# Optimization experiments

Hardware: AMD Instinct MI355X
Metric: run time of the kernel (lower is better)

Reference implementation:

```python
import jax, jax.numpy as jnp
import numpy as np

B = 16384           # number of visits (segments)
EMB = 128           # embedding dim (hardcoded in module)
HID = 64            # hidden layer size
DIAG_LEN, PROC_LEN, MED_LEN = 2000, 1500, 153


def setup_inputs() -> dict:
    key = jax.random.key(0)
    ks = jax.random.split(key, 12)
    diag_codes = jax.random.randint(ks[0], (262144,), 0, DIAG_LEN)
    diag_seg = jnp.sort(jax.random.randint(ks[1], (262144,), 0, B))
    proc_codes = jax.random.randint(ks[2], (131072,), 0, PROC_LEN)
    proc_seg = jnp.sort(jax.random.randint(ks[3], (131072,), 0, B))
    med_codes = jax.random.randint(ks[4], (196608,), 0, MED_LEN)
    med_seg = jnp.sort(jax.random.randint(ks[5], (196608,), 0, B))
    diag_table = jax.random.normal(ks[6], (DIAG_LEN, EMB), dtype=jnp.float32)
    proc_table = jax.random.normal(ks[7], (PROC_LEN, EMB), dtype=jnp.float32)
    med_table = jax.random.normal(ks[8], (MED_LEN, EMB), dtype=jnp.float32)
    W1 = jax.random.normal(ks[9], (3 * EMB, HID), dtype=jnp.float32) * 0.05
    b1 = jnp.zeros((HID,), dtype=jnp.float32)
    W2 = jax.random.normal(ks[10], (HID, MED_LEN), dtype=jnp.float32) * 0.1
    b2 = jnp.zeros((MED_LEN,), dtype=jnp.float32)
    return {
        "diag_codes": diag_codes, "diag_seg": diag_seg,
        "proc_codes": proc_codes, "proc_seg": proc_seg,
        "med_codes": med_codes, "med_seg": med_seg,
        "diag_table": diag_table, "proc_table": proc_table, "med_table": med_table,
        "W1": W1, "b1": b1, "W2": W2, "b2": b2,
    }


def _embed_sum(table, codes, seg):
    # gather [N, EMB] then segment-sum to [B, EMB] (== per-visit sum of embeddings)
    return jax.ops.segment_sum(table[codes], seg, num_segments=B)


def reference(diag_codes, diag_seg, proc_codes, proc_seg, med_codes, med_seg,
              diag_table, proc_table, med_table, W1, b1, W2, b2):
    e_diag = _embed_sum(diag_table, diag_codes, diag_seg)   # [B, 128]
    e_proc = _embed_sum(proc_table, proc_codes, proc_seg)   # [B, 128]
    e_med = _embed_sum(med_table, med_codes, med_seg)       # [B, 128]
    x = jnp.concatenate([e_diag, e_proc, e_med], axis=1)    # [B, 384]
    h = jax.nn.relu(x @ W1 + b1)                            # [B, 64]
    return jax.nn.sigmoid(h @ W2 + b2)                      # [B, med_len]
```

## Files before the change

kernel.cpp:

```cpp
#include <hip/hip_runtime.h>
#include <hip/hip_bf16.h>

#define NVIS 16384
#define EMB 128
#define HID 64
#define MED 153
#define K1 384

#define ROWS_D 2000
#define ROWS_P 1500
#define ROWS_M 153
#define RT 3653
#define TBASE_D 0
#define TBASE_P 2000
#define TBASE_M 3500
#define E8S (RT * 16)

#define W2F_OFF  0u
#define OFFS_OFF 20480u
#define OFFS_STRIDE 16388
#define TW_OFF   217136u
#define H_OFF    684720u
#define WS_NEED  (684720u + 2097152u)

#define TWB_D 500
#define TWB_P 375
#define TWB_M 39
#define TWB_ALL (TWB_D + TWB_P + TWB_M)
#define NW2F 1280

typedef float f32x4 __attribute__((ext_vector_type(4)));
typedef short s16x8 __attribute__((ext_vector_type(8)));
typedef unsigned int u32;
typedef unsigned int u32x4 __attribute__((ext_vector_type(4)));

__device__ __forceinline__ unsigned short f2bf(float f) {
  union { float f; unsigned u; } v; v.f = f;
  unsigned r = v.u + 0x7FFFu + ((v.u >> 16) & 1u);
  return (unsigned short)(r >> 16);
}

__device__ __forceinline__ void acc8m(u32x4 t, float m, float* A) {
  union { unsigned u; float f; } c;
  c.u = t[0] << 16;          A[0] = fmaf(m, c.f, A[0]);
  c.u = t[0] & 0xFFFF0000u;  A[1] = fmaf(m, c.f, A[1]);
  c.u = t[1] << 16;          A[2] = fmaf(m, c.f, A[2]);
  c.u = t[1] & 0xFFFF0000u;  A[3] = fmaf(m, c.f, A[3]);
  c.u = t[2] << 16;          A[4] = fmaf(m, c.f, A[4]);
  c.u = t[2] & 0xFFFF0000u;  A[5] = fmaf(m, c.f, A[5]);
  c.u = t[3] << 16;          A[6] = fmaf(m, c.f, A[6]);
  c.u = t[3] & 0xFFFF0000u;  A[7] = fmaf(m, c.f, A[7]);
}

__device__ __forceinline__ int lb_scalar(const int* __restrict__ a, int lo, int hi, int key) {
  while (lo < hi) {
    int mid = (lo + hi) >> 1;
    if (a[mid] < key) lo = mid + 1; else hi = mid;
  }
  return lo;
}

__device__ __forceinline__ int lb_fast_scalar(const int* __restrict__ a, int n, int key) {
  long long g = ((long long)key * (long long)n) >> 14;
  int L = (int)g - 3072, R = (int)g + 3072;
  if (L < 0) L = 0;
  if (R > n) R = n;
  const bool ok = (L == 0 || a[L - 1] < key) && (R == n || a[R] >= key);
  if (!ok) { L = 0; R = n; }
  return lb_scalar(a, L, R, key);
}

__device__ __forceinline__ int lb_wave(const int* __restrict__ a, int n, int key, int lane) {
  long long g = ((long long)key * (long long)n) >> 14;
  int L = (int)g - 3072, R = (int)g + 3072;
  if (L < 0) L = 0;
  if (R > n) R = n;
  const bool ok = (L == 0 || a[L - 1] < key) && (R == n || a[R] >= key);
  if (!ok) { L = 0; R = n; }
  int lo = L - 1, hi = R;
  while (hi - lo > 1) {
    const int width = hi - lo - 1;
    const int p = lo + 1 + (int)(((long long)width * lane) >> 6);
    const bool lt = a[p] < key;
    const unsigned long long m = __ballot(lt);
    const int t = m ? (63 - __builtin_clzll(m)) : -1;
    const int nlo = (t >= 0) ? lo + 1 + (int)(((long long)width * t) >> 6) : lo;
    const int nhi = (t < 63) ? lo + 1 + (int)(((long long)width * (t + 1)) >> 6) : hi;
    lo = nlo; hi = nhi;
  }
  return hi;
}

__global__ __launch_bounds__(256, 4) void prep_kernel(
    const int* __restrict__ diag_seg, const int* __restrict__ proc_seg,
    const int* __restrict__ med_seg,
    const float* __restrict__ dT, const float* __restrict__ pT, const float* __restrict__ mT,
    const float* __restrict__ W1, const float* __restrict__ W2,
    unsigned char* __restrict__ ws, int ND, int NP, int NM)
{
  __shared__ float w1L[128 * 64];
  const int blk = blockIdx.x;
  const int tid = threadIdx.x;
  const int totSlots = ND + NP + NM + 3;
  const int SB = (totSlots + 255) >> 8;

  if (blk < SB) {
    const int t = blk * 256 + tid;
    if (t < totSlots) {
      int T, i, n; const int* seg;
      if (t < ND + 1)           { T = 0; i = t;                 n = ND; seg = diag_seg; }
      else if (t < ND + NP + 2) { T = 1; i = t - (ND + 1);      n = NP; seg = proc_seg; }
      else                      { T = 2; i = t - (ND + NP + 2); n = NM; seg = med_seg; }
      const int prev = (i == 0) ? -1 : seg[i - 1];
      const int cur  = (i == n) ? NVIS : seg[i];
      int* o = (int*)(ws + OFFS_OFF) + T * OFFS_STRIDE;
      for (int k = prev + 1; k <= cur; ++k) o[k] = i;
    }
  } else if (blk < SB + TWB_ALL) {
    const int blk2 = blk - SB;
    const float* tbl; int rows, r0, koff, tBase;
    if (blk2 < TWB_D)              { tbl = dT; rows = ROWS_D; r0 = blk2 * 4;           koff = 0;   tBase = TBASE_D; }
    else if (blk2 < TWB_D + TWB_P) { tbl = pT; rows = ROWS_P; r0 = (blk2 - TWB_D) * 4; koff = 128; tBase = TBASE_P; }
    else                           { tbl = mT; rows = ROWS_M; r0 = (blk2 - TWB_D - TWB_P) * 4; koff = 256; tBase = TBASE_M; }
    for (int i = tid; i < 128 * 64 / 4; i += 256)
      *(f32x4*)&w1L[i * 4] = *(const f32x4*)&W1[(size_t)koff * HID + i * 4];
    __syncthreads();
    const int r = r0 + (tid >> 6);
    const int j = tid & 63;
    if (r < rows) {
      float acc = 0.f;
      #pragma unroll 8
      for (int k4 = 0; k4 < 32; ++k4) {
        const f32x4 t = *(const f32x4*)(tbl + (size_t)r * EMB + k4 * 4);
        acc += t[0] * w1L[(k4 * 4 + 0) * 64 + j] + t[1] * w1L[(k4 * 4 + 1) * 64 + j]
             + t[2] * w1L[(k4 * 4 + 2) * 64 + j] + t[3] * w1L[(k4 * 4 + 3) * 64 + j];
      }
      *(unsigned short*)(ws + TW_OFF + (size_t)(j >> 3) * E8S
                         + (size_t)(tBase + r) * 16 + (size_t)(j & 7) * 2) = f2bf(acc);
    }
  } else {
    const int t = (blk - SB - TWB_ALL) * 256 + tid;
    if (t < NW2F) {
      const int lane = t & 63, tk = t >> 6;
      const int kh = tk & 1, tile = tk >> 1;
      const int n = tile * 16 + (lane & 15);
      const int k0 = kh * 32 + (lane >> 4) * 8;
      unsigned short e0[8];
      #pragma unroll
      for (int e = 0; e < 8; ++e)
        e0[e] = (n < MED) ? f2bf(W2[(size_t)(k0 + e) * MED + n]) : (unsigned short)0;
      u32x4 o;
      o[0] = (u32)e0[0] | ((u32)e0[1] << 16);
      o[1] = (u32)e0[2] | ((u32)e0[3] << 16);
      o[2] = (u32)e0[4] | ((u32)e0[5] << 16);
      o[3] = (u32)e0[6] | ((u32)e0[7] << 16);
      *(u32x4*)(ws + W2F_OFF + (size_t)t * 16) = o;
    }
  }
}

__global__ __launch_bounds__(1024, 8) void gather8_kernel(
    const int* __restrict__ diag_codes, const int* __restrict__ proc_codes,
    const int* __restrict__ med_codes,
    const float* __restrict__ b1,
    unsigned char* __restrict__ ws)
{
  __shared__ __align__(16) u32x4 twL[RT];
  __shared__ int offsB[3][257];

  const int tid = threadIdx.x;
  const int e8 = blockIdx.x >> 6;
  const int v0 = (blockIdx.x & 63) * 256;

  const unsigned char* src = ws + TW_OFF + (size_t)e8 * E8S;
  for (int k = tid; k < RT; k += 1024)
    twL[k] = *(const u32x4*)(src + (size_t)k * 16);
  const int* offsAll = (const int*)(ws + OFFS_OFF);
  for (int t = tid; t < 3 * 257; t += 1024) {
    const int T = (t < 257) ? 0 : (t < 514) ? 1 : 2;
    const int idx = t - T * 257;
    offsB[T][idx] = offsAll[T * OFFS_STRIDE + v0 + idx];
  }
  __syncthreads();

  const int v = tid >> 2;
  const int l4 = tid & 3;
  float A[8] = {0.f, 0.f, 0.f, 0.f, 0.f, 0.f, 0.f, 0.f};

#define G8(T, CG, TBASE)                                                    \
  {                                                                         \
    const int s = offsB[T][v], e = offsB[T][v + 1];                         \
    for (int i = s + l4; i < e; i += 8) {                                   \
      const int j1 = i + 4;                                                 \
      const int i1 = (j1 < e) ? j1 : (e - 1);                               \
      const int c0 = TBASE + CG[i];                                         \
      const int c1 = TBASE + CG[i1];                                        \
      const u32x4 t0 = twL[c0];                                             \
      const u32x4 t1 = twL[c1];                                             \
      acc8m(t0, 1.f, A);                                                    \
      acc8m(t1, (j1 < e) ? 1.f : 0.f, A);                                   \
    }                                                                       \
  }
  G8(0, diag_codes, TBASE_D)
  G8(1, proc_codes, TBASE_P)
  G8(2, med_codes,  TBASE_M)
#undef G8

  #pragma unroll
  for (int d = 0; d < 8; ++d) {
    A[d] += __shfl_xor(A[d], 1);
    A[d] += __shfl_xor(A[d], 2);
  }
  if (l4 == 0) {
    const f32x4 bb0 = *(const f32x4*)(b1 + e8 * 8);
    const f32x4 bb1 = *(const f32x4*)(b1 + e8 * 8 + 4);
    u32x4 o;
    o[0] = (u32)f2bf(fmaxf(A[0] + bb0[0], 0.f)) | ((u32)f2bf(fmaxf(A[1] + bb0[1], 0.f)) << 16);
    o[1] = (u32)f2bf(fmaxf(A[2] + bb0[2], 0.f)) | ((u32)f2bf(fmaxf(A[3] + bb0[3], 0.f)) << 16);
    o[2] = (u32)f2bf(fmaxf(A[4] + bb1[0], 0.f)) | ((u32)f2bf(fmaxf(A[5] + bb1[1], 0.f)) << 16);
    o[3] = (u32)f2bf(fmaxf(A[6] + bb1[2], 0.f)) | ((u32)f2bf(fmaxf(A[7] + bb1[3], 0.f)) << 16);
    *(u32x4*)(ws + H_OFF + (size_t)(v0 + v) * 128 + e8 * 16) = o;
  }
}

__global__ __launch_bounds__(256, 8) void mlp2_kernel(
    const unsigned char* __restrict__ ws,
    const float* __restrict__ b2, float* __restrict__ out)
{
  const int tid = threadIdx.x;
  const int l = tid & 63;
  const int wv = tid >> 6;
  const int jloc = l & 15;
  const int kq = l >> 4;
  const int m0 = blockIdx.x * 16;
  const unsigned char* h = ws + H_OFF;
  const s16x8* w2f = (const s16x8*)(ws + W2F_OFF);

  const s16x8 a00 = *(const s16x8*)(h + (size_t)(m0 + jloc) * 128 + kq * 16);
  const s16x8 a01 = *(const s16x8*)(h + (size_t)(m0 + jloc) * 128 + 64 + kq * 16);

  for (int t = wv; t < 10; t += 4) {
    const int n = t * 16 + jloc;
    const bool nok = (n < MED);
    const s16x8 bw0 = w2f[(t * 2 + 0) * 64 + l];
    const s16x8 bw1 = w2f[(t * 2 + 1) * 64 + l];
    f32x4 o0 = {0.f, 0.f, 0.f, 0.f};
    o0 = __builtin_amdgcn_mfma_f32_16x16x32_bf16(a00, bw0, o0, 0, 0, 0);
    o0 = __builtin_amdgcn_mfma_f32_16x16x32_bf16(a01, bw1, o0, 0, 0, 0);
    if (nok) {
      const float bias2 = b2[n];
      #pragma unroll
      for (int r = 0; r < 4; ++r) {
        const int row = kq * 4 + r;
        const float z0 = o0[r] + bias2;
        out[(size_t)(m0 + row) * MED + n] = 1.f / (1.f + __expf(-z0));
      }
    }
  }
}

#define VPB 16
#define NTHR 512
#define NBLK (NVIS / VPB)
#define CAPD 640
#define CAPP 384
#define CAPM 512
#define CAPT_FB (CAPD + CAPP + CAPM)

__global__ __launch_bounds__(NTHR, 8) void fused_ehr_fb(
    const int* __restrict__ diag_codes, const int* __restrict__ diag_seg,
    const int* __restrict__ proc_codes, const int* __restrict__ proc_seg,
    const int* __restrict__ med_codes,  const int* __restrict__ med_seg,
    const float* __restrict__ diag_table, const float* __restrict__ proc_table,
    const float* __restrict__ med_table,
    const float* __restrict__ W1, const float* __restrict__ b1,
    const float* __restrict__ W2, const float* __restrict__ b2,
    float* __restrict__ out, int ND, int NP, int NM)
{
  __shared__ __align__(16) unsigned short xs[VPB][K1 + 8];
  __shared__ __align__(16) unsigned short hs[VPB][HID + 8];
  __shared__ int offs[3][VPB + 1];
  __shared__ int codesL[CAPT_FB];

  const int tid = threadIdx.x;
  const int l = tid & 63;
  const int wv = tid >> 6;
  const int b0 = blockIdx.x * VPB;

  if (wv < 6) {
    const int T = wv >> 1, w = wv & 1;
    const int* seg = (T == 0) ? diag_seg : (T == 1) ? proc_seg : med_seg;
    const int n = (T == 0) ? ND : (T == 1) ? NP : NM;
    const int r = lb_wave(seg, n, b0 + (w ? VPB : 0), l);
    if (l == 0) offs[T][w ? VPB : 0] = r;
  }
  __syncthreads();

  const int sD = offs[0][0], cntD = offs[0][VPB] - sD;
  const int sP = offs[1][0], cntP = offs[1][VPB] - sP;
  const int sM = offs[2][0], cntM = offs[2][VPB] - sM;
  const bool stD = (cntD <= CAPD), stP = (cntP <= CAPP), stM = (cntM <= CAPM);

  if (tid < 3 * (VPB - 1)) {
    const int T = tid / (VPB - 1), idx = tid - T * (VPB - 1) + 1;
    offs[T][idx] = offs[T][VPB];
  }
  if (stD) for (int i = tid; i < cntD; i += NTHR) codesL[i] = diag_codes[sD + i];
  if (stP) for (int i = tid; i < cntP; i += NTHR) codesL[CAPD + i] = proc_codes[sP + i];
  if (stM) for (int i = tid; i < cntM; i += NTHR) codesL[CAPD + CAPP + i] = med_codes[sM + i];
  __syncthreads();

#define MARK(Tidx, STAGED, CNT, SBASE, SEGG, NT)                                 \
  if (STAGED) {                                                                  \
    for (int i = tid; i < CNT; i += NTHR) {                                      \
      const int v1 = SEGG[SBASE + i];                                            \
      const int v0_ = (i == 0) ? (b0 - 1) : SEGG[SBASE + i - 1];                 \
      int klo = v0_ + 1; if (klo < b0 + 1) klo = b0 + 1;                         \
      int khi = v1;      if (khi > b0 + VPB - 1) khi = b0 + VPB - 1;             \
      for (int k = klo; k <= khi; ++k) offs[Tidx][k - b0] = SBASE + i;           \
    }                                                                            \
  } else if (tid < VPB - 1) {                                                    \
    offs[Tidx][tid + 1] = lb_fast_scalar(SEGG, NT, b0 + tid + 1);                \
  }

  MARK(0, stD, cntD, sD, diag_seg, ND)
  MARK(1, stP, cntP, sP, proc_seg, NP)
  MARK(2, stM, cntM, sM, med_seg,  NM)
#undef MARK
  __syncthreads();

  const int half = tid >> 5;
  const int ln = tid & 31;

#define GATH(T, CODES_G, TBL, STAGED, SGLOB, LBASE)                               \
  {                                                                               \
    const int s_ = offs[T][half], e_ = offs[T][half + 1];                         \
    float a0 = 0.f, a1 = 0.f, a2 = 0.f, a3 = 0.f;                                 \
    int i = s_;                                                                   \
    if (STAGED) {                                                                 \
      const int lb = LBASE - SGLOB;                                               \
      for (; i + 3 < e_; i += 4) {                                                \
        const int c0 = codesL[lb + i],     c1 = codesL[lb + i + 1];               \
        const int c2 = codesL[lb + i + 2], c3 = codesL[lb + i + 3];               \
        const f32x4 t0 = *(const f32x4*)(TBL + (size_t)c0 * EMB + ln * 4);        \
        const f32x4 t1 = *(const f32x4*)(TBL + (size_t)c1 * EMB + ln * 4);        \
        const f32x4 t2 = *(const f32x4*)(TBL + (size_t)c2 * EMB + ln * 4);        \
        const f32x4 t3 = *(const f32x4*)(TBL + (size_t)c3 * EMB + ln * 4);        \
        a0 += (t0[0] + t1[0]) + (t2[0] + t3[0]);                                  \
        a1 += (t0[1] + t1[1]) + (t2[1] + t3[1]);                                  \
        a2 += (t0[2] + t1[2]) + (t2[2] + t3[2]);                                  \
        a3 += (t0[3] + t1[3]) + (t2[3] + t3[3]);                                  \
      }                                                                           \
      for (; i < e_; ++i) {                                                       \
        const int c = codesL[lb + i];                                             \
        const f32x4 t = *(const f32x4*)(TBL + (size_t)c * EMB + ln * 4);          \
        a0 += t[0]; a1 += t[1]; a2 += t[2]; a3 += t[3];                           \
      }                                                                           \
    } else {                                                                      \
      for (; i < e_; ++i) {                                                       \
        const int c = CODES_G[i];                                                 \
        const f32x4 t = *(const f32x4*)(TBL + (size_t)c * EMB + ln * 4);          \
        a0 += t[0]; a1 += t[1]; a2 += t[2]; a3 += t[3];                           \
      }                                                                           \
    }                                                                             \
    const u32 p0 = (u32)f2bf(a0) | ((u32)f2bf(a1) << 16);                         \
    const u32 p1 = (u32)f2bf(a2) | ((u32)f2bf(a3) << 16);                         \
    uint2* d_ = (uint2*)&xs[half][T * EMB + ln * 4];                              \
    *d_ = make_uint2(p0, p1);                                                     \
  }

  GATH(0, diag_codes, diag_table, stD, sD, 0)
  GATH(1, proc_codes, proc_table, stP, sP, CAPD)
  GATH(2, med_codes,  med_table,  stM, sM, CAPD + CAPP)
#undef GATH
  __syncthreads();

  const int jloc = l & 15;
  const int kq = l >> 4;

  if (wv < 4) {
    const int j1 = wv * 16 + jloc;
    f32x4 acc = {0.f, 0.f, 0.f, 0.f};
    s16x8 bf;
    #pragma unroll
    for (int e = 0; e < 8; ++e)
      bf[e] = (short)f2bf(W1[(size_t)(kq * 8 + e) * HID + j1]);
    #pragma unroll
    for (int kt = 0; kt < 12; ++kt) {
      s16x8 nxt;
      if (kt < 11) {
        const int kb = (kt + 1) * 32 + kq * 8;
        #pragma unroll
        for (int e = 0; e < 8; ++e)
          nxt[e] = (short)f2bf(W1[(size_t)(kb + e) * HID + j1]);
      }
      const s16x8 a0 = *(const s16x8*)&xs[jloc][kt * 32 + kq * 8];
      acc = __builtin_amdgcn_mfma_f32_16x16x32_bf16(a0, bf, acc, 0, 0, 0);
      if (kt < 11) bf = nxt;
    }
    const float bias1 = b1[j1];
    #pragma unroll
    for (int r = 0; r < 4; ++r)
      hs[kq * 4 + r][j1] = f2bf(fmaxf(acc[r] + bias1, 0.f));
  }
  __syncthreads();

  for (int t = wv; t < 10; t += 8) {
    const int n = t * 16 + jloc;
    const bool nok = (n < MED);
    s16x8 bw0, bw1;
    #pragma unroll
    for (int e = 0; e < 8; ++e) {
      const int k0 = kq * 8 + e;
      bw0[e] = nok ? (short)f2bf(W2[(size_t)k0 * MED + n])        : (short)0;
      bw1[e] = nok ? (short)f2bf(W2[(size_t)(k0 + 32) * MED + n]) : (short)0;
    }
    f32x4 o0 = {0.f, 0.f, 0.f, 0.f};
    {
      const int ko = kq * 8;
      const s16x8 a00 = *(const s16x8*)&hs[jloc][ko];
      o0 = __builtin_amdgcn_mfma_f32_16x16x32_bf16(a00, bw0, o0, 0, 0, 0);
      const s16x8 a01 = *(const s16x8*)&hs[jloc][ko + 32];
      o0 = __builtin_amdgcn_mfma_f32_16x16x32_bf16(a01, bw1, o0, 0, 0, 0);
    }
    if (nok) {
      const float bias2 = b2[n];
      #pragma unroll
      for (int r = 0; r < 4; ++r) {
        const int row = kq * 4 + r;
        const float z0 = o0[r] + bias2;
        out[(size_t)(b0 + row) * MED + n] = 1.f / (1.f + __expf(-z0));
      }
    }
  }
}

extern "C" void kernel_launch(void* const* d_in, const int* in_sizes, int n_in,
                              void* d_out, int out_size, void* d_ws, size_t ws_size,
                              hipStream_t stream) {
  const int* diag_codes = (const int*)d_in[0];
  const int* diag_seg   = (const int*)d_in[1];
  const int* proc_codes = (const int*)d_in[2];
  const int* proc_seg   = (const int*)d_in[3];
  const int* med_codes  = (const int*)d_in[4];
  const int* med_seg    = (const int*)d_in[5];
  const float* diag_table = (const float*)d_in[6];
  const float* proc_table = (const float*)d_in[7];
  const float* med_table  = (const float*)d_in[8];
  const float* W1 = (const float*)d_in[9];
  const float* b1 = (const float*)d_in[10];
  const float* W2 = (const float*)d_in[11];
  const float* b2 = (const float*)d_in[12];
  float* out = (float*)d_out;

  const bool sizes_ok = (in_sizes[6] == ROWS_D * EMB) && (in_sizes[7] == ROWS_P * EMB)
                     && (in_sizes[8] == ROWS_M * EMB);
  if (ws_size >= WS_NEED && sizes_ok) {
    unsigned char* ws = (unsigned char*)d_ws;
    const int totSlots = in_sizes[0] + in_sizes[2] + in_sizes[4] + 3;
    const int SB = (totSlots + 255) >> 8;
    prep_kernel<<<dim3(SB + TWB_ALL + 5), dim3(256), 0, stream>>>(
        diag_seg, proc_seg, med_seg,
        diag_table, proc_table, med_table, W1, W2, ws,
        in_sizes[0], in_sizes[2], in_sizes[4]);
    gather8_kernel<<<dim3(512), dim3(1024), 0, stream>>>(
        diag_codes, proc_codes, med_codes, b1, ws);
    mlp2_kernel<<<dim3(NVIS / 16), dim3(256), 0, stream>>>(ws, b2, out);
  } else {
    fused_ehr_fb<<<dim3(NBLK), dim3(NTHR), 0, stream>>>(
        diag_codes, diag_seg, proc_codes, proc_seg, med_codes, med_seg,
        diag_table, proc_table, med_table, W1, b1, W2, b2, out,
        in_sizes[0], in_sizes[2], in_sizes[4]);
  }
}
```

Baseline: 29.51 us.

## Fuse segment gather and second MLP layer into one kernel with row-major table

Merges the gather/first-layer kernel and the MFMA second-layer kernel into a single kernel, so the hidden activations stay in shared memory and never round-trip through the workspace. This also removes one launch. The pre-multiplied table (embedding times W1) is now stored row-major in bf16 and read directly from global memory, where before each 8-column slice was staged in LDS. Each 32-lane half-wave handles one visit, with lanes split across code offsets and 8-column slices. The cost is uncached scattered global reads of the table and less code-level parallelism per visit.

New measurement: 25.62 us. 1.15x faster.

```diff
diff --git a/kernel.cpp b/kernel.cpp
--- a/kernel.cpp
+++ b/kernel.cpp
@@ -6,22 +6,22 @@
 #define HID 64
 #define MED 153
 #define K1 384
+#define VPB 16
+#define NTHR 512
+#define NBLK (NVIS / VPB)
+
+#define W2F_OFF  0u
+#define OFFS_OFF 20480u
+#define OFFS_STRIDE 16388
+#define TW_OFF   (20480u + 196656u)
+#define WS_NEED  (217136u + 467584u)
 
 #define ROWS_D 2000
 #define ROWS_P 1500
 #define ROWS_M 153
-#define RT 3653
 #define TBASE_D 0
 #define TBASE_P 2000
 #define TBASE_M 3500
-#define E8S (RT * 16)
-
-#define W2F_OFF  0u
-#define OFFS_OFF 20480u
-#define OFFS_STRIDE 16388
-#define TW_OFF   217136u
-#define H_OFF    684720u
-#define WS_NEED  (684720u + 2097152u)
 
 #define TWB_D 500
 #define TWB_P 375
@@ -135,8 +135,7 @@
         acc += t[0] * w1L[(k4 * 4 + 0) * 64 + j] + t[1] * w1L[(k4 * 4 + 1) * 64 + j]
              + t[2] * w1L[(k4 * 4 + 2) * 64 + j] + t[3] * w1L[(k4 * 4 + 3) * 64 + j];
       }
-      *(unsigned short*)(ws + TW_OFF + (size_t)(j >> 3) * E8S
-                         + (size_t)(tBase + r) * 16 + (size_t)(j & 7) * 2) = f2bf(acc);
+      *(unsigned short*)(ws + TW_OFF + (size_t)(tBase + r) * 128 + j * 2) = f2bf(acc);
     }
   } else {
     const int t = (blk - SB - TWB_ALL) * 256 + tid;
@@ -159,109 +158,120 @@
   }
 }
 
-__global__ __launch_bounds__(1024, 8) void gather8_kernel(
+__global__ __launch_bounds__(NTHR, 8) void fused_ehr_v11(
     const int* __restrict__ diag_codes, const int* __restrict__ proc_codes,
     const int* __restrict__ med_codes,
-    const float* __restrict__ b1,
-    unsigned char* __restrict__ ws)
+    const float* __restrict__ b1, const float* __restrict__ b2,
+    const unsigned char* __restrict__ ws,
+    float* __restrict__ out)
 {
-  __shared__ __align__(16) u32x4 twL[RT];
-  __shared__ int offsB[3][257];
+  __shared__ __align__(16) unsigned short hs[VPB][HID + 8];
 
   const int tid = threadIdx.x;
-  const int e8 = blockIdx.x >> 6;
-  const int v0 = (blockIdx.x & 63) * 256;
-
-  const unsigned char* src = ws + TW_OFF + (size_t)e8 * E8S;
-  for (int k = tid; k < RT; k += 1024)
-    twL[k] = *(const u32x4*)(src + (size_t)k * 16);
+  const int l = tid & 63;
+  const int wv = tid >> 6;
+  const int b0 = blockIdx.x * VPB;
   const int* offsAll = (const int*)(ws + OFFS_OFF);
-  for (int t = tid; t < 3 * 257; t += 1024) {
-    const int T = (t < 257) ? 0 : (t < 514) ? 1 : 2;
-    const int idx = t - T * 257;
-    offsB[T][idx] = offsAll[T * OFFS_STRIDE + v0 + idx];
-  }
-  __syncthreads();
-
-  const int v = tid >> 2;
-  const int l4 = tid & 3;
+
+  const int half = tid >> 5;
+  const int ln = tid & 31;
+  const int oct = ln >> 3;
+  const int sl = ln & 7;
+  const unsigned char* twb = ws + TW_OFF;
+
+  const int sD = offsAll[b0 + half];
+  const int eD = offsAll[b0 + half + 1];
+  const int sP = offsAll[OFFS_STRIDE + b0 + half];
+  const int eP = offsAll[OFFS_STRIDE + b0 + half + 1];
+  const int sM = offsAll[2 * OFFS_STRIDE + b0 + half];
+  const int eM = offsAll[2 * OFFS_STRIDE + b0 + half + 1];
+
   float A[8] = {0.f, 0.f, 0.f, 0.f, 0.f, 0.f, 0.f, 0.f};
 
-#define G8(T, CG, TBASE)                                                    \
-  {                                                                         \
-    const int s = offsB[T][v], e = offsB[T][v + 1];                         \
-    for (int i = s + l4; i < e; i += 8) {                                   \
-      const int j1 = i + 4;                                                 \
-      const int i1 = (j1 < e) ? j1 : (e - 1);                               \
-      const int c0 = TBASE + CG[i];                                         \
-      const int c1 = TBASE + CG[i1];                                        \
-      const u32x4 t0 = twL[c0];                                             \
-      const u32x4 t1 = twL[c1];                                             \
-      acc8m(t0, 1.f, A);                                                    \
-      acc8m(t1, (j1 < e) ? 1.f : 0.f, A);                                   \
-    }                                                                       \
-  }
-  G8(0, diag_codes, TBASE_D)
-  G8(1, proc_codes, TBASE_P)
-  G8(2, med_codes,  TBASE_M)
-#undef G8
+  for (int jj = sD; jj < eD; jj += 16) {
+    const int j0 = jj + oct, j1 = jj + 4 + oct, j2 = jj + 8 + oct, j3 = jj + 12 + oct;
+    const int i0 = (j0 < eD) ? j0 : (eD - 1);
+    const int i1 = (j1 < eD) ? j1 : (eD - 1);
+    const int i2 = (j2 < eD) ? j2 : (eD - 1);
+    const int i3 = (j3 < eD) ? j3 : (eD - 1);
+    const int c0 = diag_codes[i0], c1 = diag_codes[i1];
+    const int c2 = diag_codes[i2], c3 = diag_codes[i3];
+    const u32x4 t0 = *(const u32x4*)(twb + ((size_t)(TBASE_D + c0) << 7) + (sl << 4));
+    const u32x4 t1 = *(const u32x4*)(twb + ((size_t)(TBASE_D + c1) << 7) + (sl << 4));
+    const u32x4 t2 = *(const u32x4*)(twb + ((size_t)(TBASE_D + c2) << 7) + (sl << 4));
+    const u32x4 t3 = *(const u32x4*)(twb + ((size_t)(TBASE_D + c3) << 7) + (sl << 4));
+    acc8m(t0, (j0 < eD) ? 1.f : 0.f, A);
+    acc8m(t1, (j1 < eD) ? 1.f : 0.f, A);
+    acc8m(t2, (j2 < eD) ? 1.f : 0.f, A);
+    acc8m(t3, (j3 < eD) ? 1.f : 0.f, A);
+  }
+  for (int jj = sP; jj < eP; jj += 8) {
+    const int j0 = jj + oct, j1 = jj + 4 + oct;
+    const int i0 = (j0 < eP) ? j0 : (eP - 1);
+    const int i1 = (j1 < eP) ? j1 : (eP - 1);
+    const int c0 = proc_codes[i0], c1 = proc_codes[i1];
+    const u32x4 t0 = *(const u32x4*)(twb + ((size_t)(TBASE_P + c0) << 7) + (sl << 4));
+    const u32x4 t1 = *(const u32x4*)(twb + ((size_t)(TBASE_P + c1) << 7) + (sl << 4));
+    acc8m(t0, (j0 < eP) ? 1.f : 0.f, A);
+    acc8m(t1, (j1 < eP) ? 1.f : 0.f, A);
+  }
+  for (int jj = sM; jj < eM; jj += 8) {
+    const int j0 = jj + oct, j1 = jj + 4 + oct;
+    const int i0 = (j0 < eM) ? j0 : (eM - 1);
+    const int i1 = (j1 < eM) ? j1 : (eM - 1);
+    const int c0 = med_codes[i0], c1 = med_codes[i1];
+    const u32x4 t0 = *(const u32x4*)(twb + ((size_t)(TBASE_M + c0) << 7) + (sl << 4));
+    const u32x4 t1 = *(const u32x4*)(twb + ((size_t)(TBASE_M + c1) << 7) + (sl << 4));
+    acc8m(t0, (j0 < eM) ? 1.f : 0.f, A);
+    acc8m(t1, (j1 < eM) ? 1.f : 0.f, A);
+  }
 
   #pragma unroll
   for (int d = 0; d < 8; ++d) {
-    A[d] += __shfl_xor(A[d], 1);
-    A[d] += __shfl_xor(A[d], 2);
-  }
-  if (l4 == 0) {
-    const f32x4 bb0 = *(const f32x4*)(b1 + e8 * 8);
-    const f32x4 bb1 = *(const f32x4*)(b1 + e8 * 8 + 4);
+    A[d] += __shfl_xor(A[d], 8);
+    A[d] += __shfl_xor(A[d], 16);
+  }
+  if (ln < 8) {
+    const f32x4 bb0 = *(const f32x4*)(b1 + sl * 8);
+    const f32x4 bb1 = *(const f32x4*)(b1 + sl * 8 + 4);
     u32x4 o;
     o[0] = (u32)f2bf(fmaxf(A[0] + bb0[0], 0.f)) | ((u32)f2bf(fmaxf(A[1] + bb0[1], 0.f)) << 16);
     o[1] = (u32)f2bf(fmaxf(A[2] + bb0[2], 0.f)) | ((u32)f2bf(fmaxf(A[3] + bb0[3], 0.f)) << 16);
     o[2] = (u32)f2bf(fmaxf(A[4] + bb1[0], 0.f)) | ((u32)f2bf(fmaxf(A[5] + bb1[1], 0.f)) << 16);
     o[3] = (u32)f2bf(fmaxf(A[6] + bb1[2], 0.f)) | ((u32)f2bf(fmaxf(A[7] + bb1[3], 0.f)) << 16);
-    *(u32x4*)(ws + H_OFF + (size_t)(v0 + v) * 128 + e8 * 16) = o;
-  }
-}
-
-__global__ __launch_bounds__(256, 8) void mlp2_kernel(
-    const unsigned char* __restrict__ ws,
-    const float* __restrict__ b2, float* __restrict__ out)
-{
-  const int tid = threadIdx.x;
-  const int l = tid & 63;
-  const int wv = tid >> 6;
+    *(u32x4*)&hs[half][sl * 8] = o;
+  }
+  __syncthreads();
+
   const int jloc = l & 15;
   const int kq = l >> 4;
-  const int m0 = blockIdx.x * 16;
-  const unsigned char* h = ws + H_OFF;
   const s16x8* w2f = (const s16x8*)(ws + W2F_OFF);
 
-  const s16x8 a00 = *(const s16x8*)(h + (size_t)(m0 + jloc) * 128 + kq * 16);
-  const s16x8 a01 = *(const s16x8*)(h + (size_t)(m0 + jloc) * 128 + 64 + kq * 16);
-
-  for (int t = wv; t < 10; t += 4) {
+  for (int t = wv; t < 10; t += 8) {
     const int n = t * 16 + jloc;
     const bool nok = (n < MED);
     const s16x8 bw0 = w2f[(t * 2 + 0) * 64 + l];
     const s16x8 bw1 = w2f[(t * 2 + 1) * 64 + l];
     f32x4 o0 = {0.f, 0.f, 0.f, 0.f};
-    o0 = __builtin_amdgcn_mfma_f32_16x16x32_bf16(a00, bw0, o0, 0, 0, 0);
-    o0 = __builtin_amdgcn_mfma_f32_16x16x32_bf16(a01, bw1, o0, 0, 0, 0);
+    {
+      const int ko = kq * 8;
+      const s16x8 a00 = *(const s16x8*)&hs[jloc][ko];
+      o0 = __builtin_amdgcn_mfma_f32_16x16x32_bf16(a00, bw0, o0, 0, 0, 0);
+      const s16x8 a01 = *(const s16x8*)&hs[jloc][ko + 32];
+      o0 = __builtin_amdgcn_mfma_f32_16x16x32_bf16(a01, bw1, o0, 0, 0, 0);
+    }
     if (nok) {
       const float bias2 = b2[n];
       #pragma unroll
       for (int r = 0; r < 4; ++r) {
         const int row = kq * 4 + r;
         const float z0 = o0[r] + bias2;
-        out[(size_t)(m0 + row) * MED + n] = 1.f / (1.f + __expf(-z0));
+        out[(size_t)(b0 + row) * MED + n] = 1.f / (1.f + __expf(-z0));
       }
     }
   }
 }
 
-#define VPB 16
-#define NTHR 512
-#define NBLK (NVIS / VPB)
 #define CAPD 640
 #define CAPP 384
 #define CAPM 512
@@ -463,9 +473,8 @@
         diag_seg, proc_seg, med_seg,
         diag_table, proc_table, med_table, W1, W2, ws,
         in_sizes[0], in_sizes[2], in_sizes[4]);
-    gather8_kernel<<<dim3(512), dim3(1024), 0, stream>>>(
-        diag_codes, proc_codes, med_codes, b1, ws);
-    mlp2_kernel<<<dim3(NVIS / 16), dim3(256), 0, stream>>>(ws, b2, out);
+    fused_ehr_v11<<<dim3(NBLK), dim3(NTHR), 0, stream>>>(
+        diag_codes, proc_codes, med_codes, b1, b2, ws, out);
   } else {
     fused_ehr_fb<<<dim3(NBLK), dim3(NTHR), 0, stream>>>(
         diag_codes, diag_seg, proc_codes, proc_seg, med_codes, med_seg,
```
